# Kernel tuning notes

Measured on AMD Instinct MI355X. Metric: run time of the kernel, lower is better.

Reference implementation:

```python
import jax, jax.numpy as jnp
import numpy as np

KERNEL = 500
PAD_IDX = 256


def setup_inputs() -> dict:
    key = jax.random.key(0)
    ks = jax.random.split(key, 8)
    B, L = 8, 1_000_000
    x = jax.random.randint(ks[0], (B, L), 0, 257, dtype=jnp.int64)
    emb = jax.random.normal(ks[1], (257, 8), dtype=jnp.float32)
    emb = emb.at[PAD_IDX].set(0.0)  # padding_idx row is zero
    W1 = jax.random.normal(ks[2], (128, 8, KERNEL), dtype=jnp.float32) * 0.02
    b1 = jax.random.normal(ks[3], (128,), dtype=jnp.float32) * 0.02
    W2 = jax.random.normal(ks[4], (128, 8, KERNEL), dtype=jnp.float32) * 0.02
    b2 = jax.random.normal(ks[5], (128,), dtype=jnp.float32) * 0.02
    fcW = jax.random.normal(ks[6], (2, 128), dtype=jnp.float32) * 0.1
    fcb = jax.random.normal(ks[7], (2,), dtype=jnp.float32) * 0.1
    return {"x": x, "emb": emb, "W1": W1, "b1": b1, "W2": W2, "b2": b2, "fcW": fcW, "fcb": fcb}


def reference(x, emb, W1, b1, W2, b2, fcW, fcb):
    B, L = x.shape
    P = L // KERNEL  # non-overlapping patches (stride == kernel_size)
    # embedding with padding_idx semantics: output zero at pad positions
    e = emb[x] * (x != PAD_IDX)[..., None].astype(emb.dtype)  # [B, L, 8]
    patches = e.reshape(B, P, KERNEL, 8)                      # [B, P, K, C]
    # conv1d(k=stride=500) == patchified GEMM; weight layout [out, in, k]
    g1 = jnp.einsum('bpkc,ock->bpo', patches, W1) + b1        # [B, P, 128]
    g2 = jnp.einsum('bpkc,ock->bpo', patches, W2) + b2
    h = jax.nn.relu(g1 * jax.nn.sigmoid(g2))                  # GLU gate + relu
    m = jnp.max(h, axis=1)                                    # global max pool -> [B, 128]
    return m @ fcW.T + fcb                                    # [B, num_classes]
```

## Files before the change

kernel.cpp:

```cpp
#include <hip/hip_runtime.h>


typedef __attribute__((ext_vector_type(8))) short short8;
typedef __attribute__((ext_vector_type(4))) float f32x4;

__device__ __forceinline__ unsigned short f2b(float f) {
    union { float f; unsigned u; } un;
    un.f = f;
    unsigned u = un.u;
    return (unsigned short)((u + 0x7FFFu + ((u >> 16) & 1u)) >> 16);
}

#define KT_COUNT 125
#define WS_BBLK_BYTES (KT_COUNT * 256 * 32 * 2)
#define WS_MWS_OFF WS_BBLK_BYTES

__global__ __launch_bounds__(256) void prep_weights(
        const float* __restrict__ W1, const float* __restrict__ W2,
        unsigned short* __restrict__ Bblk, float* __restrict__ m_ws) {
    int u   = blockIdx.x * 256 + threadIdx.x;
    int kt  = u >> 10;
    int rem = u & 1023;
    int o   = rem >> 2;
    int g   = rem & 3;
    int k   = kt * 4 + g;
    const float* W = (o < 128) ? W1 : W2;
    int oo = o & 127;
    unsigned short v[8];
#pragma unroll
    for (int c = 0; c < 8; ++c) v[c] = f2b(W[oo * 4000 + c * 500 + k]);
    uint4 pack;
    pack.x = (unsigned)v[0] | ((unsigned)v[1] << 16);
    pack.y = (unsigned)v[2] | ((unsigned)v[3] << 16);
    pack.z = (unsigned)v[4] | ((unsigned)v[5] << 16);
    pack.w = (unsigned)v[6] | ((unsigned)v[7] << 16);
    *(uint4*)&Bblk[u * 8] = pack;
    if (blockIdx.x < 4) m_ws[blockIdx.x * 256 + threadIdx.x] = 0.f;
}

__global__ __launch_bounds__(512, 2) void malconv_main(
        const int* __restrict__ x, const float* __restrict__ emb,
        const float* __restrict__ b1, const float* __restrict__ b2,
        const unsigned short* __restrict__ Bblk, float* __restrict__ m_ws) {
    __shared__ __align__(16) unsigned short embb[257 * 8];
    __shared__ __align__(16) unsigned short Alds[2][64 * 40];
    __shared__ float g2_lds[64 * 132];

    const int t = threadIdx.x;
    for (int e = t; e < 257 * 8; e += 512) embb[e] = f2b(emb[e]);

    const int m0   = blockIdx.x * 64;
    const int lane = t & 63, wave = t >> 6;
    const int quad = lane >> 4, l16 = lane & 15;
    const int mq   = wave >> 2, nq = wave & 3;

    const unsigned short* bbase = Bblk + (nq * 64 + l16) * 32 + quad * 8;

    f32x4 acc[2][4];
#pragma unroll
    for (int mi = 0; mi < 2; ++mi)
#pragma unroll
        for (int ni = 0; ni < 4; ++ni) {
            f32x4 z = {0.f, 0.f, 0.f, 0.f};
            acc[mi][ni] = z;
        }

    const int ai = t >> 2, aj = t & 3;
    const int* xptr = x + (m0 + ai) * 500 + aj;

    __syncthreads();

    int xvn = 0;
    if (t < 256) {
        int xv = xptr[0];
        *(uint4*)&Alds[0][ai * 40 + aj * 8] = *(const uint4*)&embb[xv * 8];
        xvn = xptr[4];
    }
    short8 bcur[4], bnxt[4];
#pragma unroll
    for (int ni = 0; ni < 4; ++ni)
        bcur[ni] = *(const short8*)(bbase + ni * 512);
    __syncthreads();

    for (int kt = 0; kt < KT_COUNT; ++kt) {
        const int cur = kt & 1;
        if (kt < KT_COUNT - 1) {
#pragma unroll
            for (int ni = 0; ni < 4; ++ni)
                bnxt[ni] = *(const short8*)(bbase + (kt + 1) * 8192 + ni * 512);
        }
        short8 afrag[2];
#pragma unroll
        for (int mi = 0; mi < 2; ++mi)
            afrag[mi] = *(const short8*)
                &Alds[cur][(mq * 32 + mi * 16 + l16) * 40 + quad * 8];
        if (t < 256 && kt < KT_COUNT - 1) {
            *(uint4*)&Alds[cur ^ 1][ai * 40 + aj * 8] =
                *(const uint4*)&embb[xvn * 8];
            if (kt < KT_COUNT - 2) xvn = xptr[(kt + 2) * 4];
        }
#pragma unroll
        for (int mi = 0; mi < 2; ++mi)
#pragma unroll
            for (int ni = 0; ni < 4; ++ni)
                acc[mi][ni] = __builtin_amdgcn_mfma_f32_16x16x32_bf16(
                    afrag[mi], bcur[ni], acc[mi][ni], 0, 0, 0);
#pragma unroll
        for (int ni = 0; ni < 4; ++ni) bcur[ni] = bnxt[ni];
        __syncthreads();
    }

    if (nq >= 2) {
#pragma unroll
        for (int mi = 0; mi < 2; ++mi)
#pragma unroll
            for (int ni = 0; ni < 4; ++ni)
#pragma unroll
                for (int r = 0; r < 4; ++r)
                    g2_lds[(mq * 32 + mi * 16 + quad * 4 + r) * 132 +
                           (nq - 2) * 64 + ni * 16 + l16] = acc[mi][ni][r];
    }
    __syncthreads();
    if (nq < 2) {
        const int b0 = m0 / 2000;
        const int bsplit = (b0 + 1) * 2000;
        const bool crosses = (m0 + 63) >= bsplit;
#pragma unroll
        for (int ni = 0; ni < 4; ++ni) {
            int o = nq * 64 + ni * 16 + l16;
            float bb1 = b1[o], bb2 = b2[o];
            float mx0 = 0.f, mx1 = 0.f;
#pragma unroll
            for (int mi = 0; mi < 2; ++mi)
#pragma unroll
                for (int r = 0; r < 4; ++r) {
                    int ml = mq * 32 + mi * 16 + quad * 4 + r;
                    float g1 = acc[mi][ni][r] + bb1;
                    float g2 = g2_lds[ml * 132 + o] + bb2;
                    float h = fmaxf(g1 / (1.f + __expf(-g2)), 0.f);
                    if (m0 + ml >= bsplit) mx1 = fmaxf(mx1, h);
                    else                   mx0 = fmaxf(mx0, h);
                }
            mx0 = fmaxf(mx0, __shfl_xor(mx0, 16));
            mx0 = fmaxf(mx0, __shfl_xor(mx0, 32));
            mx1 = fmaxf(mx1, __shfl_xor(mx1, 16));
            mx1 = fmaxf(mx1, __shfl_xor(mx1, 32));
            if (quad == 0) {
                atomicMax((int*)&m_ws[b0 * 128 + o], __float_as_int(mx0));
                if (crosses)
                    atomicMax((int*)&m_ws[(b0 + 1) * 128 + o], __float_as_int(mx1));
            }
        }
    }
}

__global__ void fc_kernel(const float* __restrict__ m_ws,
                          const float* __restrict__ fcW,
                          const float* __restrict__ fcb,
                          float* __restrict__ out) {
    int t = threadIdx.x;
    if (t < 16) {
        int b = t >> 1, j = t & 1;
        float s = 0.f;
        for (int o = 0; o < 128; ++o) s += m_ws[b * 128 + o] * fcW[j * 128 + o];
        out[t] = s + fcb[j];
    }
}

extern "C" void kernel_launch(void* const* d_in, const int* in_sizes, int n_in,
                              void* d_out, int out_size, void* d_ws, size_t ws_size,
                              hipStream_t stream) {
    const int*   x   = (const int*)d_in[0];
    const float* emb = (const float*)d_in[1];
    const float* W1  = (const float*)d_in[2];
    const float* b1  = (const float*)d_in[3];
    const float* W2  = (const float*)d_in[4];
    const float* b2  = (const float*)d_in[5];
    const float* fcW = (const float*)d_in[6];
    const float* fcb = (const float*)d_in[7];
    float* out = (float*)d_out;

    unsigned short* Bblk = (unsigned short*)d_ws;
    float* m_ws = (float*)((char*)d_ws + WS_MWS_OFF);

    prep_weights<<<500, 256, 0, stream>>>(W1, W2, Bblk, m_ws);
    malconv_main<<<250, 512, 0, stream>>>(x, emb, b1, b2, Bblk, m_ws);
    fc_kernel<<<1, 64, 0, stream>>>(m_ws, fcW, fcb, out);
}
```

Before: 150.1 us.

## Gather A fragments directly from LDS embedding table and remove per-step barriers

```diff
diff --git a/kernel.cpp b/kernel.cpp
--- a/kernel.cpp
+++ b/kernel.cpp
@@ -43,18 +43,20 @@
         const float* __restrict__ b1, const float* __restrict__ b2,
         const unsigned short* __restrict__ Bblk, float* __restrict__ m_ws) {
     __shared__ __align__(16) unsigned short embb[257 * 8];
-    __shared__ __align__(16) unsigned short Alds[2][64 * 40];
-    __shared__ float g2_lds[64 * 132];
 
     const int t = threadIdx.x;
     for (int e = t; e < 257 * 8; e += 512) embb[e] = f2b(emb[e]);
+    __syncthreads();
 
     const int m0   = blockIdx.x * 64;
     const int lane = t & 63, wave = t >> 6;
     const int quad = lane >> 4, l16 = lane & 15;
     const int mq   = wave >> 2, nq = wave & 3;
 
-    const unsigned short* bbase = Bblk + (nq * 64 + l16) * 32 + quad * 8;
+    const int* xp0 = x + (m0 + mq * 32 + l16) * 500 + quad;
+    const int* xp1 = xp0 + 16 * 500;
+
+    const unsigned short* bbase = Bblk + (nq * 32 + l16) * 32 + quad * 8;
 
     f32x4 acc[2][4];
 #pragma unroll
@@ -65,91 +67,67 @@
             acc[mi][ni] = z;
         }
 
-    const int ai = t >> 2, aj = t & 3;
-    const int* xptr = x + (m0 + ai) * 500 + aj;
+    int xc0 = xp0[0], xc1 = xp1[0];
+    int xn0 = xp0[4], xn1 = xp1[4];
+    short8 bcur[4];
+    bcur[0] = *(const short8*)(bbase);
+    bcur[1] = *(const short8*)(bbase + 512);
+    bcur[2] = *(const short8*)(bbase + 4096);
+    bcur[3] = *(const short8*)(bbase + 4608);
 
-    __syncthreads();
+#pragma unroll 5
+    for (int kt = 0; kt < KT_COUNT; ++kt) {
+        int ktf = kt + 2; if (ktf > KT_COUNT - 1) ktf = KT_COUNT - 1;
+        int ktb = kt + 1; if (ktb > KT_COUNT - 1) ktb = KT_COUNT - 1;
+        int xf0 = xp0[ktf * 4];
+        int xf1 = xp1[ktf * 4];
+        const unsigned short* bb = bbase + ktb * 8192;
+        short8 bnxt[4];
+        bnxt[0] = *(const short8*)(bb);
+        bnxt[1] = *(const short8*)(bb + 512);
+        bnxt[2] = *(const short8*)(bb + 4096);
+        bnxt[3] = *(const short8*)(bb + 4608);
+        short8 a0 = *(const short8*)&embb[xc0 * 8];
+        short8 a1 = *(const short8*)&embb[xc1 * 8];
+#pragma unroll
+        for (int ni = 0; ni < 4; ++ni) {
+            acc[0][ni] = __builtin_amdgcn_mfma_f32_16x16x32_bf16(
+                a0, bcur[ni], acc[0][ni], 0, 0, 0);
+            acc[1][ni] = __builtin_amdgcn_mfma_f32_16x16x32_bf16(
+                a1, bcur[ni], acc[1][ni], 0, 0, 0);
+        }
+        xc0 = xn0; xc1 = xn1; xn0 = xf0; xn1 = xf1;
+#pragma unroll
+        for (int ni = 0; ni < 4; ++ni) bcur[ni] = bnxt[ni];
+    }
 
-    int xvn = 0;
-    if (t < 256) {
-        int xv = xptr[0];
-        *(uint4*)&Alds[0][ai * 40 + aj * 8] = *(const uint4*)&embb[xv * 8];
-        xvn = xptr[4];
-    }
-    short8 bcur[4], bnxt[4];
+    const int b0 = m0 / 2000;
+    const int bsplit = (b0 + 1) * 2000;
+    const bool crosses = (m0 + 63) >= bsplit;
 #pragma unroll
-    for (int ni = 0; ni < 4; ++ni)
-        bcur[ni] = *(const short8*)(bbase + ni * 512);
-    __syncthreads();
-
-    for (int kt = 0; kt < KT_COUNT; ++kt) {
-        const int cur = kt & 1;
-        if (kt < KT_COUNT - 1) {
-#pragma unroll
-            for (int ni = 0; ni < 4; ++ni)
-                bnxt[ni] = *(const short8*)(bbase + (kt + 1) * 8192 + ni * 512);
-        }
-        short8 afrag[2];
-#pragma unroll
-        for (int mi = 0; mi < 2; ++mi)
-            afrag[mi] = *(const short8*)
-                &Alds[cur][(mq * 32 + mi * 16 + l16) * 40 + quad * 8];
-        if (t < 256 && kt < KT_COUNT - 1) {
-            *(uint4*)&Alds[cur ^ 1][ai * 40 + aj * 8] =
-                *(const uint4*)&embb[xvn * 8];
-            if (kt < KT_COUNT - 2) xvn = xptr[(kt + 2) * 4];
-        }
+    for (int ni = 0; ni < 2; ++ni) {
+        int o = nq * 32 + ni * 16 + l16;
+        float bb1 = b1[o], bb2 = b2[o];
+        float mx0 = 0.f, mx1 = 0.f;
 #pragma unroll
         for (int mi = 0; mi < 2; ++mi)
 #pragma unroll
-            for (int ni = 0; ni < 4; ++ni)
-                acc[mi][ni] = __builtin_amdgcn_mfma_f32_16x16x32_bf16(
-                    afrag[mi], bcur[ni], acc[mi][ni], 0, 0, 0);
-#pragma unroll
-        for (int ni = 0; ni < 4; ++ni) bcur[ni] = bnxt[ni];
-        __syncthreads();
-    }
-
-    if (nq >= 2) {
-#pragma unroll
-        for (int mi = 0; mi < 2; ++mi)
-#pragma unroll
-            for (int ni = 0; ni < 4; ++ni)
-#pragma unroll
-                for (int r = 0; r < 4; ++r)
-                    g2_lds[(mq * 32 + mi * 16 + quad * 4 + r) * 132 +
-                           (nq - 2) * 64 + ni * 16 + l16] = acc[mi][ni][r];
-    }
-    __syncthreads();
-    if (nq < 2) {
-        const int b0 = m0 / 2000;
-        const int bsplit = (b0 + 1) * 2000;
-        const bool crosses = (m0 + 63) >= bsplit;
-#pragma unroll
-        for (int ni = 0; ni < 4; ++ni) {
-            int o = nq * 64 + ni * 16 + l16;
-            float bb1 = b1[o], bb2 = b2[o];
-            float mx0 = 0.f, mx1 = 0.f;
-#pragma unroll
-            for (int mi = 0; mi < 2; ++mi)
-#pragma unroll
-                for (int r = 0; r < 4; ++r) {
-                    int ml = mq * 32 + mi * 16 + quad * 4 + r;
-                    float g1 = acc[mi][ni][r] + bb1;
-                    float g2 = g2_lds[ml * 132 + o] + bb2;
-                    float h = fmaxf(g1 / (1.f + __expf(-g2)), 0.f);
-                    if (m0 + ml >= bsplit) mx1 = fmaxf(mx1, h);
-                    else                   mx0 = fmaxf(mx0, h);
-                }
-            mx0 = fmaxf(mx0, __shfl_xor(mx0, 16));
-            mx0 = fmaxf(mx0, __shfl_xor(mx0, 32));
-            mx1 = fmaxf(mx1, __shfl_xor(mx1, 16));
-            mx1 = fmaxf(mx1, __shfl_xor(mx1, 32));
-            if (quad == 0) {
-                atomicMax((int*)&m_ws[b0 * 128 + o], __float_as_int(mx0));
-                if (crosses)
-                    atomicMax((int*)&m_ws[(b0 + 1) * 128 + o], __float_as_int(mx1));
+            for (int r = 0; r < 4; ++r) {
+                int ml = mq * 32 + mi * 16 + quad * 4 + r;
+                float g1 = acc[mi][ni][r] + bb1;
+                float g2 = acc[mi][ni + 2][r] + bb2;
+                float h = fmaxf(g1 / (1.f + __expf(-g2)), 0.f);
+                if (m0 + ml >= bsplit) mx1 = fmaxf(mx1, h);
+                else                   mx0 = fmaxf(mx0, h);
             }
+        mx0 = fmaxf(mx0, __shfl_xor(mx0, 16));
+        mx0 = fmaxf(mx0, __shfl_xor(mx0, 32));
+        mx1 = fmaxf(mx1, __shfl_xor(mx1, 16));
+        mx1 = fmaxf(mx1, __shfl_xor(mx1, 32));
+        if (quad == 0) {
+            atomicMax((int*)&m_ws[b0 * 128 + o], __float_as_int(mx0));
+            if (crosses)
+                atomicMax((int*)&m_ws[(b0 + 1) * 128 + o], __float_as_int(mx1));
         }
     }
 }
```

After: 174.1 us. +16.0%, slower.
